# Optimization experiments

Hardware: AMD Instinct MI355X
Metric: run time of the kernel (lower is better)

Reference implementation:

```python
import jax, jax.numpy as jnp
import numpy as np

N_NODES = 100000
N_EDGES = 1600000
F_IN = 128
HID = 128
N_LAYERS = 4
N_CLASSES = 10
N_GRAPHS = 512
BN_EPS = 1e-5


def setup_inputs() -> dict:
    key = jax.random.key(0)
    ks = jax.random.split(key, 16)
    x = jax.random.normal(ks[0], (N_NODES, F_IN), dtype=jnp.float32)
    edge_index = jax.random.randint(ks[1], (2, N_EDGES), 0, N_NODES, dtype=jnp.int64)
    edge_attr = jax.random.normal(ks[2], (N_EDGES, 8), dtype=jnp.float32)
    batch = jnp.sort(jax.random.randint(ks[3], (N_NODES,), 0, N_GRAPHS, dtype=jnp.int64))
    # Per-layer MLP params (in-dim is 128 for all layers since F_IN == HID).
    s1 = 1.0 / np.sqrt(F_IN)
    s2 = 1.0 / np.sqrt(2 * HID)
    W1 = jax.random.uniform(ks[4], (N_LAYERS, F_IN, 2 * HID), minval=-s1, maxval=s1, dtype=jnp.float32)
    b1 = jax.random.uniform(ks[5], (N_LAYERS, 2 * HID), minval=-s1, maxval=s1, dtype=jnp.float32)
    gamma1 = jnp.ones((N_LAYERS, 2 * HID), dtype=jnp.float32)
    beta1 = jnp.zeros((N_LAYERS, 2 * HID), dtype=jnp.float32)
    W2 = jax.random.uniform(ks[6], (N_LAYERS, 2 * HID, HID), minval=-s2, maxval=s2, dtype=jnp.float32)
    b2 = jax.random.uniform(ks[7], (N_LAYERS, HID), minval=-s2, maxval=s2, dtype=jnp.float32)
    sf = 1.0 / np.sqrt(HID * N_LAYERS)
    fcW = jax.random.uniform(ks[8], (HID * N_LAYERS, N_CLASSES), minval=-sf, maxval=sf, dtype=jnp.float32)
    fcb = jax.random.uniform(ks[9], (N_CLASSES,), minval=-sf, maxval=sf, dtype=jnp.float32)
    return {"x": x, "edge_index": edge_index, "edge_attr": edge_attr, "batch": batch,
            "W1": W1, "b1": b1, "gamma1": gamma1, "beta1": beta1,
            "W2": W2, "b2": b2, "fcW": fcW, "fcb": fcb}


def reference(x, edge_index, edge_attr, batch, W1, b1, gamma1, beta1, W2, b2, fcW, fcb):
    # edge_attr is unused by the original forward.
    src, dst = edge_index[0], edge_index[1]
    n = x.shape[0]
    # In-degree for mean aggregation (messages flow src -> dst in PyG).
    deg = jax.ops.segment_sum(jnp.ones((src.shape[0],), x.dtype), dst, num_segments=n)
    inv_deg = 1.0 / jnp.maximum(deg, 1.0)
    h = x
    xs = []
    for i in range(N_LAYERS):
        # GINConv, eps=0, aggr='mean': nn(x + mean_j h_j)
        agg = jax.ops.segment_sum(h[src], dst, num_segments=n) * inv_deg[:, None]
        z = h + agg
        z = z @ W1[i] + b1[i]                      # [N, 2H]
        mu = jnp.mean(z, axis=0)
        var = jnp.mean(jnp.square(z - mu), axis=0)  # biased var (BN training mode)
        z = gamma1[i] * (z - mu) * jax.lax.rsqrt(var + BN_EPS) + beta1[i]
        z = jax.nn.relu(z)
        z = z @ W2[i] + b2[i]                      # [N, H]
        h = jax.nn.relu(z)
        xs.append(h)
    xcat = jnp.concatenate(xs, axis=1)             # [N, H*L]
    # global_mean_pool over graph ids
    gsum = jax.ops.segment_sum(xcat, batch, num_segments=N_GRAPHS)
    gcnt = jax.ops.segment_sum(jnp.ones((n,), xcat.dtype), batch, num_segments=N_GRAPHS)
    pooled = gsum / jnp.maximum(gcnt, 1.0)[:, None]
    logits = pooled @ fcW + fcb
    return jax.nn.log_softmax(logits, axis=-1)
```

## Files before the change

### kernel.cpp

```cpp
#include <hip/hip_runtime.h>
#include <cstdint>
#include <cstddef>

#define NN 100000
#define NE 1600000
#define FD 128
#define HD2 256
#define NLAYERS 4
#define NGR 512
#define NCLS 10
#define BNEPS 1e-5f
#define G1TILES 1563
#define GEMM_GRID 521
#define EB 6250
#define NB 391
#define NSLICE 8
#define SLICEW 12500

typedef unsigned short ushort_t;
typedef short bf16x8 __attribute__((ext_vector_type(8)));
typedef float f32x4 __attribute__((ext_vector_type(4)));

__device__ __forceinline__ float bfl(unsigned short u) {
  unsigned v = ((unsigned)u) << 16;
  return __builtin_bit_cast(float, v);
}
__device__ __forceinline__ unsigned short fbf(float f) {
  unsigned u = __builtin_bit_cast(unsigned, f);
  unsigned r = (u + 0x7FFFu + ((u >> 16) & 1u)) >> 16;
  return (unsigned short)r;
}

__global__ void k_init_detect(const int* ei, int* flag, int* degi) {
  int i = blockIdx.x * 256 + threadIdx.x;
  if (i < NN) degi[i] = 0;
  if (blockIdx.x == 0) {
    __shared__ int nz;
    if (threadIdx.x == 0) nz = 0;
    __syncthreads();
    if (ei[2 * threadIdx.x + 1] != 0) atomicAdd(&nz, 1);
    __syncthreads();
    if (threadIdx.x == 0) flag[0] = (nz == 0) ? 1 : 0;
  }
}

__global__ void k_repack_deg(const int* ei, const int* batch, const int* flag,
                             int* src32, int* dst32, int* batch32, int* degi) {
  int i = blockIdx.x * 256 + threadIdx.x;
  const bool wide = (flag[0] != 0);
  if (i < NE) {
    int s = wide ? ei[2 * i] : ei[i];
    int d = wide ? ei[2 * (NE + i)] : ei[NE + i];
    src32[i] = s;
    dst32[i] = d;
    atomicAdd(&degi[d], 1);
  }
  if (i < NN) batch32[i] = wide ? batch[2 * i] : batch[i];
}

__global__ void k_scan1(const int* degi, int* rowptr, int* bsum) {
  __shared__ int s[256];
  int t = threadIdx.x;
  int i = blockIdx.x * 256 + t;
  int v = (i < NN) ? degi[i] : 0;
  s[t] = v;
  __syncthreads();
  for (int off = 1; off < 256; off <<= 1) {
    int x = (t >= off) ? s[t - off] : 0;
    __syncthreads();
    s[t] += x;
    __syncthreads();
  }
  if (i < NN) rowptr[i] = s[t] - v;
  if (t == 255) bsum[blockIdx.x] = s[255];
}

__global__ void k_scan2_gstats(int* bsum, int nb, const int* __restrict__ batch,
                               int* __restrict__ gstart, int* __restrict__ gcnti) {
  __shared__ int s[512];
  int t = threadIdx.x;
  int v = (t < nb) ? bsum[t] : 0;
  s[t] = v;
  __syncthreads();
  for (int off = 1; off < 512; off <<= 1) {
    int x = (t >= off) ? s[t - off] : 0;
    __syncthreads();
    s[t] += x;
    __syncthreads();
  }
  if (t < nb) bsum[t] = s[t] - v;
  if (t < NGR) {
    int g = t;
    int lo = 0, hi = NN;
    while (lo < hi) { int m = (lo + hi) >> 1; if (batch[m] < g) lo = m + 1; else hi = m; }
    int st = lo;
    hi = NN;
    while (lo < hi) { int m = (lo + hi) >> 1; if (batch[m] < g + 1) lo = m + 1; else hi = m; }
    gstart[g] = st;
    gcnti[g] = lo - st;
  }
}

__global__ void k_scan3_cursor(int* rowptr, const int* bsum, int* cursor,
                               const int* degi, float* inv_deg) {
  int i = blockIdx.x * 256 + threadIdx.x;
  if (i < NN) {
    int r = rowptr[i] + bsum[blockIdx.x];
    rowptr[i] = r;
    cursor[i] = r;
    inv_deg[i] = 1.f / fmaxf((float)degi[i], 1.f);
  }
  if (i == 0) rowptr[NN] = NE;
}

__global__ void k_scatter8(const int* __restrict__ src, const int* __restrict__ dst,
                           int* cursor, int* csr) {
  int slice = blockIdx.x & (NSLICE - 1);
  int e = (blockIdx.x >> 3) * 256 + threadIdx.x;
  if (e >= NE) return;
  int d = dst[e];
  int lo = slice * SLICEW;
  if (d >= lo && d < lo + SLICEW) {
    int p = atomicAdd(&cursor[d], 1);
    csr[p] = src[e];
  }
}

__global__ void k_cvt_x(const float* __restrict__ x, ushort_t* __restrict__ xb) {
  int i = blockIdx.x * 256 + threadIdx.x;
  if (i >= NN * FD / 8) return;
  const float4* p = (const float4*)x + (size_t)i * 2;
  float4 a = p[0], b = p[1];
  bf16x8 o;
  o[0] = (short)fbf(a.x); o[1] = (short)fbf(a.y);
  o[2] = (short)fbf(a.z); o[3] = (short)fbf(a.w);
  o[4] = (short)fbf(b.x); o[5] = (short)fbf(b.y);
  o[6] = (short)fbf(b.z); o[7] = (short)fbf(b.w);
  *(bf16x8*)&xb[(size_t)i * 8] = o;
}

__global__ void k_cvt_w(const float* __restrict__ W1, const float* __restrict__ W2,
                        ushort_t* __restrict__ W1t, ushort_t* __restrict__ W2t) {
  int idx = blockIdx.x * 256 + threadIdx.x;
  if (idx >= NLAYERS * FD * HD2) return;
  int l = idx >> 15, r = idx & 32767;
  {
    int n = r >> 7, k = r & 127;
    W1t[(size_t)l * 32768 + n * 128 + k] = fbf(W1[(size_t)l * 32768 + k * 256 + n]);
  }
  {
    int n = r >> 8, k = r & 255;
    W2t[(size_t)l * 32768 + n * 256 + k] = fbf(W2[(size_t)l * 32768 + k * 128 + n]);
  }
}

__global__ void k_agg(const ushort_t* __restrict__ h, const int* __restrict__ rowptr,
                      const int* __restrict__ csr, const float* __restrict__ inv_deg,
                      ushort_t* __restrict__ tout, float* bnsum) {
  if (blockIdx.x == 0) {
    bnsum[threadIdx.x] = 0.f;
    bnsum[HD2 + threadIdx.x] = 0.f;
  }
  const int wave = threadIdx.x >> 6;
  const int lane = threadIdx.x & 63;
  const int half = lane >> 5, sub = lane & 31;
  const int node = blockIdx.x * 8 + wave * 2 + half;
  const uint2* h4 = (const uint2*)h;
  int beg = rowptr[node];
  int deg = rowptr[node + 1] - beg;
  int maxd = max(deg, __shfl_xor(deg, 32));
  float a0 = 0.f, a1 = 0.f, a2 = 0.f, a3 = 0.f;
  int j = 0;
  for (; j + 8 <= maxd; j += 8) {
    uint2 p[8];
#pragma unroll
    for (int u = 0; u < 8; ++u) {
      bool valid = (j + u) < deg;
      int idx = beg + (valid ? j + u : 0);
      int s = csr[idx];
      uint2 v = h4[(size_t)s * 32 + sub];
      p[u].x = valid ? v.x : 0u;
      p[u].y = valid ? v.y : 0u;
    }
#pragma unroll
    for (int u = 0; u < 8; ++u) {
      a0 += bfl((unsigned short)(p[u].x & 0xFFFF));
      a1 += bfl((unsigned short)(p[u].x >> 16));
      a2 += bfl((unsigned short)(p[u].y & 0xFFFF));
      a3 += bfl((unsigned short)(p[u].y >> 16));
    }
  }
  for (; j < maxd; ++j) {
    bool valid = j < deg;
    int idx = beg + (valid ? j : 0);
    int s = csr[idx];
    uint2 v = h4[(size_t)s * 32 + sub];
    if (valid) {
      a0 += bfl((unsigned short)(v.x & 0xFFFF));
      a1 += bfl((unsigned short)(v.x >> 16));
      a2 += bfl((unsigned short)(v.y & 0xFFFF));
      a3 += bfl((unsigned short)(v.y >> 16));
    }
  }
  float id = inv_deg[node];
  uint2 c = h4[(size_t)node * 32 + sub];
  float o0 = bfl((unsigned short)(c.x & 0xFFFF)) + a0 * id;
  float o1 = bfl((unsigned short)(c.x >> 16)) + a1 * id;
  float o2 = bfl((unsigned short)(c.y & 0xFFFF)) + a2 * id;
  float o3 = bfl((unsigned short)(c.y >> 16)) + a3 * id;
  uint2 ow;
  ow.x = (unsigned)fbf(o0) | ((unsigned)fbf(o1) << 16);
  ow.y = (unsigned)fbf(o2) | ((unsigned)fbf(o3) << 16);
  ((uint2*)tout)[(size_t)node * 32 + sub] = ow;
}

__launch_bounds__(256, 2)
__global__ void k_gemm1(const ushort_t* __restrict__ A, const ushort_t* __restrict__ Bt,
                        const float* __restrict__ bias, ushort_t* __restrict__ Z,
                        float* __restrict__ bnsum) {
  __shared__ ushort_t Bs[256 * 128];
  __shared__ ushort_t As[64 * 128];
  const int tid = threadIdx.x;
#pragma unroll
  for (int i = 0; i < 16; ++i) {
    int chunk = tid + 256 * i;
    int n = chunk >> 4, c = chunk & 15;
    bf16x8 v = *(const bf16x8*)&Bt[n * 128 + c * 8];
    *(bf16x8*)((char*)Bs + n * 256 + ((c * 16) ^ ((n & 7) << 4))) = v;
  }
  const int wv = tid >> 6, ln = tid & 63;
  const int lr = ln & 15, lg = ln >> 4;
  float bb[16];
#pragma unroll
  for (int nt = 0; nt < 16; ++nt) bb[nt] = bias[nt * 16 + lr];
  float s0[16] = {}, s1[16] = {};

  for (int t = blockIdx.x; t < G1TILES; t += GEMM_GRID) {
    int row0 = t * 64;
#pragma unroll
    for (int i = 0; i < 4; ++i) {
      int chunk = tid + 256 * i;
      int r = chunk >> 4, c = chunk & 15;
      int grow = row0 + r; if (grow >= NN) grow = NN - 1;
      bf16x8 v = *(const bf16x8*)&A[(size_t)grow * FD + c * 8];
      *(bf16x8*)((char*)As + r * 256 + ((c * 16) ^ ((r & 7) << 4))) = v;
    }
    __syncthreads();
    int arow = wv * 16 + lr;
    bf16x8 af[4];
#pragma unroll
    for (int ks = 0; ks < 4; ++ks)
      af[ks] = *(bf16x8*)((char*)As + arow * 256 + ((ks * 64 + lg * 16) ^ ((arow & 7) << 4)));
    f32x4 acc[16];
#pragma unroll
    for (int nt = 0; nt < 16; ++nt) acc[nt] = (f32x4){0.f, 0.f, 0.f, 0.f};
#pragma unroll
    for (int nt = 0; nt < 16; ++nt) {
      int bn = nt * 16 + lr;
#pragma unroll
      for (int ks = 0; ks < 4; ++ks) {
        bf16x8 bfr = *(bf16x8*)((char*)Bs + bn * 256 + ((ks * 64 + lg * 16) ^ ((bn & 7) << 4)));
        acc[nt] = __builtin_amdgcn_mfma_f32_16x16x32_bf16(af[ks], bfr, acc[nt], 0, 0, 0);
      }
    }
    __syncthreads();
#pragma unroll
    for (int nt = 0; nt < 16; ++nt) {
      int col = nt * 16 + lr;
#pragma unroll
      for (int j = 0; j < 4; ++j) {
        int grow = row0 + wv * 16 + lg * 4 + j;
        if (grow < NN) {
          unsigned short zb = fbf(acc[nt][j] + bb[nt]);
          Z[(size_t)grow * HD2 + col] = zb;
          float zf = bfl(zb);
          s0[nt] += zf;
          s1[nt] += zf * zf;
        }
      }
    }
  }
  __syncthreads();
  float* ls = (float*)As;
  ls[tid] = 0.f; ls[tid + 256] = 0.f;
  __syncthreads();
#pragma unroll
  for (int nt = 0; nt < 16; ++nt) {
    int col = nt * 16 + lr;
    atomicAdd(&ls[col], s0[nt]);
    atomicAdd(&ls[col + 256], s1[nt]);
  }
  __syncthreads();
  if (tid < 256) {
    atomicAdd(&bnsum[tid], ls[tid]);
    atomicAdd(&bnsum[HD2 + tid], ls[tid + 256]);
  }
}

__global__ void k_bnfin(const float* bnsum, const float* gamma, const float* beta, float* a12) {
  int c = threadIdx.x;
  if (c < HD2) {
    float mu = bnsum[c] * (1.f / (float)NN);
    float var = fmaxf(bnsum[HD2 + c] * (1.f / (float)NN) - mu * mu, 0.f);
    float rs = rsqrtf(var + BNEPS);
    float g = gamma[c] * rs;
    a12[c] = g;
    a12[HD2 + c] = beta[c] - mu * g;
  }
}

__launch_bounds__(256, 2)
__global__ void k_gemm2(const ushort_t* __restrict__ Zin, const ushort_t* __restrict__ Bt,
                        const float* __restrict__ bias, const float* __restrict__ a12,
                        ushort_t* __restrict__ Hout) {
  __shared__ ushort_t Bs[128 * 256];
  __shared__ ushort_t As[64 * 128];
  const int tid = threadIdx.x;
#pragma unroll
  for (int i = 0; i < 16; ++i) {
    int chunk = tid + 256 * i;
    int n = chunk >> 5, c = chunk & 31;
    bf16x8 v = *(const bf16x8*)&Bt[n * 256 + c * 8];
    *(bf16x8*)((char*)Bs + n * 512 + ((c * 16) ^ ((n & 7) << 4))) = v;
  }
  const int wv = tid >> 6, ln = tid & 63;
  const int lr = ln & 15, lg = ln >> 4;
  float a1v[2][8], a2v[2][8];
#pragma unroll
  for (int h = 0; h < 2; ++h)
#pragma unroll
    for (int j = 0; j < 8; ++j) {
      int k = h * 128 + (tid & 15) * 8 + j;
      a1v[h][j] = a12[k];
      a2v[h][j] = a12[HD2 + k];
    }
  float bb[8];
#pragma unroll
  for (int nt = 0; nt < 8; ++nt) bb[nt] = bias[nt * 16 + lr];

  for (int t = blockIdx.x; t < G1TILES; t += GEMM_GRID) {
    int row0 = t * 64;
    f32x4 acc[8];
#pragma unroll
    for (int nt = 0; nt < 8; ++nt) acc[nt] = (f32x4){0.f, 0.f, 0.f, 0.f};
#pragma unroll
    for (int h = 0; h < 2; ++h) {
#pragma unroll
      for (int i = 0; i < 4; ++i) {
        int chunk = tid + 256 * i;
        int r = chunk >> 4, c = chunk & 15;
        int grow = row0 + r; if (grow >= NN) grow = NN - 1;
        bf16x8 v = *(const bf16x8*)&Zin[(size_t)grow * HD2 + h * 128 + c * 8];
        bf16x8 o;
#pragma unroll
        for (int j = 0; j < 8; ++j) {
          float f = bfl((unsigned short)v[j]) * a1v[h][j] + a2v[h][j];
          o[j] = (short)fbf(fmaxf(f, 0.f));
        }
        *(bf16x8*)((char*)As + r * 256 + ((c * 16) ^ ((r & 7) << 4))) = o;
      }
      __syncthreads();
      int arow = wv * 16 + lr;
      bf16x8 af[4];
#pragma unroll
      for (int ks = 0; ks < 4; ++ks)
        af[ks] = *(bf16x8*)((char*)As + arow * 256 + ((ks * 64 + lg * 16) ^ ((arow & 7) << 4)));
#pragma unroll
      for (int nt = 0; nt < 8; ++nt) {
        int bn = nt * 16 + lr;
#pragma unroll
        for (int ks = 0; ks < 4; ++ks) {
          bf16x8 bfr = *(bf16x8*)((char*)Bs + bn * 512 +
                                  (((h * 16 + ks * 4 + lg) * 16) ^ ((bn & 7) << 4)));
          acc[nt] = __builtin_amdgcn_mfma_f32_16x16x32_bf16(af[ks], bfr, acc[nt], 0, 0, 0);
        }
      }
      __syncthreads();
    }
#pragma unroll
    for (int nt = 0; nt < 8; ++nt) {
      int col = nt * 16 + lr;
#pragma unroll
      for (int j = 0; j < 4; ++j) {
        int grow = row0 + wv * 16 + lg * 4 + j;
        if (grow < NN) Hout[(size_t)grow * FD + col] = fbf(fmaxf(acc[nt][j] + bb[nt], 0.f));
      }
    }
  }
}

__launch_bounds__(256)
__global__ void k_pool_fc(const ushort_t* __restrict__ hb, const int* __restrict__ gstart,
                          const int* __restrict__ gcnti, const float* __restrict__ fcW,
                          const float* __restrict__ fcb, float* __restrict__ out) {
  __shared__ float pool4[4][512];
  __shared__ float wred[4][NCLS];
  int g = blockIdx.x, t = threadIdx.x;
  int start = gstart[g], cnt = gcnti[g];
  int chunk = t & 63, ro = t >> 6;
  int L = chunk >> 4, cc = (chunk & 15) * 8;
  const ushort_t* hL = hb + (size_t)L * NN * FD;
  float s[8] = {};
  for (int r = start + ro; r < start + cnt; r += 4) {
    bf16x8 v = *(const bf16x8*)&hL[(size_t)r * FD + cc];
#pragma unroll
    for (int j = 0; j < 8; ++j) s[j] += bfl((unsigned short)v[j]);
  }
#pragma unroll
  for (int j = 0; j < 8; ++j) pool4[ro][chunk * 8 + j] = s[j];
  __syncthreads();
  float inv = 1.f / fmaxf((float)cnt, 1.f);
  float pA = (pool4[0][t] + pool4[1][t] + pool4[2][t] + pool4[3][t]) * inv;
  float pB = (pool4[0][t + 256] + pool4[1][t + 256] + pool4[2][t + 256] + pool4[3][t + 256]) * inv;
  float pacc[NCLS];
#pragma unroll
  for (int c = 0; c < NCLS; ++c)
    pacc[c] = pA * fcW[t * NCLS + c] + pB * fcW[(t + 256) * NCLS + c];
#pragma unroll
  for (int off = 32; off > 0; off >>= 1)
#pragma unroll
    for (int c = 0; c < NCLS; ++c) pacc[c] += __shfl_down(pacc[c], off);
  if ((t & 63) == 0)
#pragma unroll
    for (int c = 0; c < NCLS; ++c) wred[t >> 6][c] = pacc[c];
  __syncthreads();
  if (t == 0) {
    float lg[NCLS];
    float mx = -1e30f;
#pragma unroll
    for (int c = 0; c < NCLS; ++c) {
      lg[c] = wred[0][c] + wred[1][c] + wred[2][c] + wred[3][c] + fcb[c];
      mx = fmaxf(mx, lg[c]);
    }
    float se = 0.f;
#pragma unroll
    for (int c = 0; c < NCLS; ++c) se += expf(lg[c] - mx);
    float lse = mx + logf(se);
#pragma unroll
    for (int c = 0; c < NCLS; ++c) out[(size_t)g * NCLS + c] = lg[c] - lse;
  }
}

extern "C" void kernel_launch(void* const* d_in, const int* in_sizes, int n_in,
                              void* d_out, int out_size, void* d_ws, size_t ws_size,
                              hipStream_t stream) {
  const float* x      = (const float*)d_in[0];
  const int*   ei     = (const int*)d_in[1];
  const int*   batch  = (const int*)d_in[3];
  const float* W1     = (const float*)d_in[4];
  const float* b1     = (const float*)d_in[5];
  const float* gamma1 = (const float*)d_in[6];
  const float* beta1  = (const float*)d_in[7];
  const float* W2     = (const float*)d_in[8];
  const float* b2     = (const float*)d_in[9];
  const float* fcW    = (const float*)d_in[10];
  const float* fcb    = (const float*)d_in[11];
  float* out = (float*)d_out;

  char* p = (char*)d_ws;
  auto alloc = [&](size_t bytes) {
    char* r = p;
    p += (bytes + 255) & ~(size_t)255;
    return r;
  };
  ushort_t* xbf   = (ushort_t*)alloc((size_t)NN * FD * 2);
  ushort_t* tbuf  = (ushort_t*)alloc((size_t)NN * FD * 2);
  ushort_t* Zbuf  = (ushort_t*)alloc((size_t)NN * HD2 * 2);
  ushort_t* hb    = (ushort_t*)alloc((size_t)NLAYERS * NN * FD * 2);
  ushort_t* W1t   = (ushort_t*)alloc((size_t)NLAYERS * FD * HD2 * 2);
  ushort_t* W2t   = (ushort_t*)alloc((size_t)NLAYERS * FD * HD2 * 2);
  float* inv_deg  = (float*)alloc((size_t)NN * 4);
  float* bnsum    = (float*)alloc(2 * HD2 * 4);
  float* a12      = (float*)alloc(2 * HD2 * 4);
  int* degi       = (int*)alloc((size_t)NN * 4);
  int* rowptr     = (int*)alloc((size_t)(NN + 1) * 4);
  int* cursor     = (int*)alloc((size_t)NN * 4);
  int* csr        = (int*)alloc((size_t)NE * 4);
  int* bsum       = (int*)alloc(512 * 4);
  int* src32      = (int*)alloc((size_t)NE * 4);
  int* dst32      = (int*)alloc((size_t)NE * 4);
  int* batch32    = (int*)alloc((size_t)NN * 4);
  int* gcnti      = (int*)alloc((size_t)NGR * 4);
  int* gstart     = (int*)alloc((size_t)NGR * 4);
  int* flag       = (int*)alloc(256);

  k_init_detect<<<NB, 256, 0, stream>>>(ei, flag, degi);
  k_repack_deg<<<EB, 256, 0, stream>>>(ei, batch, flag, src32, dst32, batch32, degi);
  k_scan1<<<NB, 256, 0, stream>>>(degi, rowptr, bsum);
  k_scan2_gstats<<<1, 512, 0, stream>>>(bsum, NB, batch32, gstart, gcnti);
  k_scan3_cursor<<<NB, 256, 0, stream>>>(rowptr, bsum, cursor, degi, inv_deg);
  k_scatter8<<<EB * NSLICE, 256, 0, stream>>>(src32, dst32, cursor, csr);
  k_cvt_x<<<(NN * FD / 8 + 255) / 256, 256, 0, stream>>>(x, xbf);
  k_cvt_w<<<(NLAYERS * FD * HD2 + 255) / 256, 256, 0, stream>>>(W1, W2, W1t, W2t);

  const ushort_t* hin = xbf;
  for (int L = 0; L < NLAYERS; ++L) {
    k_agg<<<NN / 8, 256, 0, stream>>>(hin, rowptr, csr, inv_deg, tbuf, bnsum);
    k_gemm1<<<GEMM_GRID, 256, 0, stream>>>(tbuf, W1t + (size_t)L * FD * HD2,
                                           b1 + (size_t)L * HD2, Zbuf, bnsum);
    k_bnfin<<<1, 256, 0, stream>>>(bnsum, gamma1 + (size_t)L * HD2, beta1 + (size_t)L * HD2, a12);
    k_gemm2<<<GEMM_GRID, 256, 0, stream>>>(Zbuf, W2t + (size_t)L * FD * HD2,
                                           b2 + (size_t)L * FD, a12,
                                           hb + (size_t)L * NN * FD);
    hin = hb + (size_t)L * NN * FD;
  }
  k_pool_fc<<<NGR, 256, 0, stream>>>(hb, gstart, gcnti, fcW, fcb, out);
}
```

Before: 832.7 us.

## Pre-swizzle weights and aggregation output for direct global-to-LDS loads, fuse BN finalize

Weights and the aggregation output tensor are now written to global memory already in the XOR-swizzled LDS layout, so the GEMM kernels can fill shared memory with global_load_lds DMA instead of loading through registers and storing. The separate BN finalize kernel is removed and its work is folded into the gemm2 prologue, where each block recomputes the scale and shift from bnsum. The aggregation buffer is padded by 64 rows so the last tile can be read without clamping. The risk is that gemm1's A load still relies on the swizzle laid down by k_agg and on correct padding, and that gemm2 redundantly recomputes the BN coefficients in every block.

New measurement: 867.3 us. 4.2% more time.

```diff
diff --git a/kernel.cpp b/kernel.cpp
--- a/kernel.cpp
+++ b/kernel.cpp
@@ -31,6 +31,12 @@
   return (unsigned short)r;
 }
 
+typedef const unsigned __attribute__((address_space(1)))* gas_t;
+typedef unsigned __attribute__((address_space(3)))* las_t;
+__device__ __forceinline__ void gload16(const void* g, void* l) {
+  __builtin_amdgcn_global_load_lds((gas_t)g, (las_t)l, 16, 0, 0);
+}
+
 __global__ void k_init_detect(const int* ei, int* flag, int* degi) {
   int i = blockIdx.x * 256 + threadIdx.x;
   if (i < NN) degi[i] = 0;
@@ -140,17 +146,25 @@
 }
 
 __global__ void k_cvt_w(const float* __restrict__ W1, const float* __restrict__ W2,
-                        ushort_t* __restrict__ W1t, ushort_t* __restrict__ W2t) {
+                        ushort_t* __restrict__ W1s, ushort_t* __restrict__ W2s) {
   int idx = blockIdx.x * 256 + threadIdx.x;
-  if (idx >= NLAYERS * FD * HD2) return;
-  int l = idx >> 15, r = idx & 32767;
+  if (idx >= NLAYERS * 4096) return;
+  int l = idx >> 12, rem = idx & 4095;
   {
-    int n = r >> 7, k = r & 127;
-    W1t[(size_t)l * 32768 + n * 128 + k] = fbf(W1[(size_t)l * 32768 + k * 256 + n]);
+    int n = rem >> 4, c = rem & 15;
+    bf16x8 o;
+#pragma unroll
+    for (int j = 0; j < 8; ++j)
+      o[j] = (short)fbf(W1[(size_t)l * 32768 + (size_t)(c * 8 + j) * 256 + n]);
+    *(bf16x8*)((char*)W1s + (size_t)l * 65536 + n * 256 + ((c * 16) ^ ((n & 7) << 4))) = o;
   }
   {
-    int n = r >> 8, k = r & 255;
-    W2t[(size_t)l * 32768 + n * 256 + k] = fbf(W2[(size_t)l * 32768 + k * 128 + n]);
+    int n = rem >> 5, c = rem & 31;
+    bf16x8 o;
+#pragma unroll
+    for (int j = 0; j < 8; ++j)
+      o[j] = (short)fbf(W2[(size_t)l * 32768 + (size_t)(c * 8 + j) * 128 + n]);
+    *(bf16x8*)((char*)W2s + (size_t)l * 65536 + n * 512 + ((c * 16) ^ ((n & 7) << 4))) = o;
   }
 }
 
@@ -211,7 +225,8 @@
   uint2 ow;
   ow.x = (unsigned)fbf(o0) | ((unsigned)fbf(o1) << 16);
   ow.y = (unsigned)fbf(o2) | ((unsigned)fbf(o3) << 16);
-  ((uint2*)tout)[(size_t)node * 32 + sub] = ow;
+  unsigned swoff = (((unsigned)(sub >> 1) * 16) ^ (((unsigned)node & 7) << 4)) + (sub & 1) * 8;
+  *(uint2*)((char*)tout + (size_t)node * 256 + swoff) = ow;
 }
 
 __launch_bounds__(256, 2)
@@ -221,13 +236,10 @@
   __shared__ ushort_t Bs[256 * 128];
   __shared__ ushort_t As[64 * 128];
   const int tid = threadIdx.x;
-#pragma unroll
-  for (int i = 0; i < 16; ++i) {
-    int chunk = tid + 256 * i;
-    int n = chunk >> 4, c = chunk & 15;
-    bf16x8 v = *(const bf16x8*)&Bt[n * 128 + c * 8];
-    *(bf16x8*)((char*)Bs + n * 256 + ((c * 16) ^ ((n & 7) << 4))) = v;
-  }
+  const int wslot = (tid & ~63) * 16;
+#pragma unroll
+  for (int i = 0; i < 16; ++i)
+    gload16((const char*)Bt + (size_t)(i * 256 + tid) * 16, (char*)Bs + i * 4096 + wslot);
   const int wv = tid >> 6, ln = tid & 63;
   const int lr = ln & 15, lg = ln >> 4;
   float bb[16];
@@ -237,14 +249,10 @@
 
   for (int t = blockIdx.x; t < G1TILES; t += GEMM_GRID) {
     int row0 = t * 64;
-#pragma unroll
-    for (int i = 0; i < 4; ++i) {
-      int chunk = tid + 256 * i;
-      int r = chunk >> 4, c = chunk & 15;
-      int grow = row0 + r; if (grow >= NN) grow = NN - 1;
-      bf16x8 v = *(const bf16x8*)&A[(size_t)grow * FD + c * 8];
-      *(bf16x8*)((char*)As + r * 256 + ((c * 16) ^ ((r & 7) << 4))) = v;
-    }
+    const char* Ag = (const char*)A + (size_t)row0 * 256;
+#pragma unroll
+    for (int i = 0; i < 4; ++i)
+      gload16(Ag + (size_t)(i * 256 + tid) * 16, (char*)As + i * 4096 + wslot);
     __syncthreads();
     int arow = wv * 16 + lr;
     bf16x8 af[4];
@@ -297,32 +305,28 @@
   }
 }
 
-__global__ void k_bnfin(const float* bnsum, const float* gamma, const float* beta, float* a12) {
-  int c = threadIdx.x;
-  if (c < HD2) {
-    float mu = bnsum[c] * (1.f / (float)NN);
-    float var = fmaxf(bnsum[HD2 + c] * (1.f / (float)NN) - mu * mu, 0.f);
-    float rs = rsqrtf(var + BNEPS);
-    float g = gamma[c] * rs;
-    a12[c] = g;
-    a12[HD2 + c] = beta[c] - mu * g;
-  }
-}
-
 __launch_bounds__(256, 2)
 __global__ void k_gemm2(const ushort_t* __restrict__ Zin, const ushort_t* __restrict__ Bt,
-                        const float* __restrict__ bias, const float* __restrict__ a12,
+                        const float* __restrict__ bias, const float* __restrict__ bnsum,
+                        const float* __restrict__ gamma, const float* __restrict__ beta,
                         ushort_t* __restrict__ Hout) {
   __shared__ ushort_t Bs[128 * 256];
   __shared__ ushort_t As[64 * 128];
+  __shared__ float sa1[HD2], sa2[HD2];
   const int tid = threadIdx.x;
-#pragma unroll
-  for (int i = 0; i < 16; ++i) {
-    int chunk = tid + 256 * i;
-    int n = chunk >> 5, c = chunk & 31;
-    bf16x8 v = *(const bf16x8*)&Bt[n * 256 + c * 8];
-    *(bf16x8*)((char*)Bs + n * 512 + ((c * 16) ^ ((n & 7) << 4))) = v;
-  }
+  const int wslot = (tid & ~63) * 16;
+  {
+    float mu = bnsum[tid] * (1.f / (float)NN);
+    float var = fmaxf(bnsum[HD2 + tid] * (1.f / (float)NN) - mu * mu, 0.f);
+    float rs = rsqrtf(var + BNEPS);
+    float g = gamma[tid] * rs;
+    sa1[tid] = g;
+    sa2[tid] = beta[tid] - mu * g;
+  }
+#pragma unroll
+  for (int i = 0; i < 16; ++i)
+    gload16((const char*)Bt + (size_t)(i * 256 + tid) * 16, (char*)Bs + i * 4096 + wslot);
+  __syncthreads();
   const int wv = tid >> 6, ln = tid & 63;
   const int lr = ln & 15, lg = ln >> 4;
   float a1v[2][8], a2v[2][8];
@@ -331,8 +335,8 @@
 #pragma unroll
     for (int j = 0; j < 8; ++j) {
       int k = h * 128 + (tid & 15) * 8 + j;
-      a1v[h][j] = a12[k];
-      a2v[h][j] = a12[HD2 + k];
+      a1v[h][j] = sa1[k];
+      a2v[h][j] = sa2[k];
     }
   float bb[8];
 #pragma unroll
@@ -464,14 +468,13 @@
     return r;
   };
   ushort_t* xbf   = (ushort_t*)alloc((size_t)NN * FD * 2);
-  ushort_t* tbuf  = (ushort_t*)alloc((size_t)NN * FD * 2);
+  ushort_t* tbuf  = (ushort_t*)alloc((size_t)(NN + 64) * FD * 2);
   ushort_t* Zbuf  = (ushort_t*)alloc((size_t)NN * HD2 * 2);
   ushort_t* hb    = (ushort_t*)alloc((size_t)NLAYERS * NN * FD * 2);
   ushort_t* W1t   = (ushort_t*)alloc((size_t)NLAYERS * FD * HD2 * 2);
   ushort_t* W2t   = (ushort_t*)alloc((size_t)NLAYERS * FD * HD2 * 2);
   float* inv_deg  = (float*)alloc((size_t)NN * 4);
   float* bnsum    = (float*)alloc(2 * HD2 * 4);
-  float* a12      = (float*)alloc(2 * HD2 * 4);
   int* degi       = (int*)alloc((size_t)NN * 4);
   int* rowptr     = (int*)alloc((size_t)(NN + 1) * 4);
   int* cursor     = (int*)alloc((size_t)NN * 4);
@@ -491,16 +494,16 @@
   k_scan3_cursor<<<NB, 256, 0, stream>>>(rowptr, bsum, cursor, degi, inv_deg);
   k_scatter8<<<EB * NSLICE, 256, 0, stream>>>(src32, dst32, cursor, csr);
   k_cvt_x<<<(NN * FD / 8 + 255) / 256, 256, 0, stream>>>(x, xbf);
-  k_cvt_w<<<(NLAYERS * FD * HD2 + 255) / 256, 256, 0, stream>>>(W1, W2, W1t, W2t);
+  k_cvt_w<<<(NLAYERS * 4096 + 255) / 256, 256, 0, stream>>>(W1, W2, W1t, W2t);
 
   const ushort_t* hin = xbf;
   for (int L = 0; L < NLAYERS; ++L) {
     k_agg<<<NN / 8, 256, 0, stream>>>(hin, rowptr, csr, inv_deg, tbuf, bnsum);
     k_gemm1<<<GEMM_GRID, 256, 0, stream>>>(tbuf, W1t + (size_t)L * FD * HD2,
                                            b1 + (size_t)L * HD2, Zbuf, bnsum);
-    k_bnfin<<<1, 256, 0, stream>>>(bnsum, gamma1 + (size_t)L * HD2, beta1 + (size_t)L * HD2, a12);
     k_gemm2<<<GEMM_GRID, 256, 0, stream>>>(Zbuf, W2t + (size_t)L * FD * HD2,
-                                           b2 + (size_t)L * FD, a12,
+                                           b2 + (size_t)L * FD, bnsum,
+                                           gamma1 + (size_t)L * HD2, beta1 + (size_t)L * HD2,
                                            hb + (size_t)L * NN * FD);
     hin = hb + (size_t)L * NN * FD;
   }
```
